# Kernel tuning notes

Hardware: AMD Instinct MI355X
Metric: run time of the kernel (lower is better)

The kernel has to match this reference:

```python
import jax, jax.numpy as jnp
import numpy as np

NUM_BANDS = 30
NUM_CH = 128
DIFF_HEAD_DIM = NUM_CH // 4 // 2  # 16
GRAPH_HEADS = 4
GRAPH_HD = NUM_CH // GRAPH_HEADS  # 32
SCALES = [2, 4, 8, 16, 32]


def _band_config():
    widths = np.array([2,3,3,3,3,3,3,3,3,3,3,8,8,8,8,8,8,8,8,8,8,8,8,16,16,16,16,16,16,16,17], dtype=np.float64)
    starts = np.concatenate([[0.0], np.cumsum(widths)])[:NUM_BANDS]
    freqs = (starts + widths[:NUM_BANDS] / 2.0) * 31.25
    slot = {2: 0, 4: 1, 8: 2, 16: 3, 32: 4}
    scale_slots, init_w = [], []
    for f in freqs:
        if f < 500:
            sc, iw = [8, 16, 32], [0.1, 0.3, 0.6]
        elif f < 2000:
            sc, iw = [4, 8, 16], [0.3, 0.4, 0.3]
        else:
            sc, iw = [2, 4, 8], [0.6, 0.3, 0.1]
        scale_slots.append([slot[s] for s in sc])
        init_w.append(iw)
    return freqs, np.array(scale_slots, np.int32), np.array(init_w, np.float32)

BAND_FREQS, SCALE_SLOTS, INIT_W = _band_config()


def setup_inputs() -> dict:
    key = jax.random.key(0)
    ks = iter(jax.random.split(key, 64))
    B, N, T, K = 4, NUM_CH, 512, NUM_BANDS

    def nrm(shape, fan):
        return jax.random.normal(next(ks), shape, jnp.float32) / np.sqrt(fan)

    inp = {}
    inp['x'] = jax.random.normal(next(ks), (B, N, T, K), jnp.float32)
    # per-band differential attention weights (stored [in, out])
    inp['Wq'] = nrm((K, N, N), N)
    inp['Wk'] = nrm((K, N, N), N)
    inp['Wv'] = nrm((K, N, N // 2), N)
    inp['Wo'] = nrm((K, N // 2, N), N // 2)
    inp['bo'] = jnp.zeros((K, N), jnp.float32)
    # per-band lambda predictors
    inp['lw1'] = nrm((K, 8, 16), 8)
    inp['lb1'] = jnp.zeros((K, 16), jnp.float32)
    inp['lw2'] = nrm((K, 16, 1), 16)
    inp['lb2'] = jnp.zeros((K, 1), jnp.float32)
    # shared multiscale conv kernels (torch OIH layout)
    for s in SCALES:
        inp[f'cw{s}'] = nrm((N, N, s), N * s)
        inp[f'cb{s}'] = jnp.zeros((N,), jnp.float32)
    inp['fusion_w'] = jnp.asarray(INIT_W)
    inp['band_embed'] = jnp.log(jnp.asarray(BAND_FREQS, jnp.float32) + 1.0)[:, None] * jax.random.normal(next(ks), (K, 64), jnp.float32) * 0.1
    # graph attention weights
    inp['gWq'] = nrm((N, N), N); inp['gbq'] = jnp.zeros((N,), jnp.float32)
    inp['gWk'] = nrm((N, N), N); inp['gbk'] = jnp.zeros((N,), jnp.float32)
    inp['gWv'] = nrm((N, N), N); inp['gbv'] = jnp.zeros((N,), jnp.float32)
    inp['gWo'] = nrm((N, N), N); inp['gbo'] = jnp.zeros((N,), jnp.float32)
    return inp


def reference(x, Wq, Wk, Wv, Wo, bo, lw1, lb1, lw2, lb2,
              cw2, cb2, cw4, cb4, cw8, cb8, cw16, cb16, cw32, cb32,
              fusion_w, band_embed, gWq, gbq, gWk, gbk, gWv, gbv, gWo, gbo):
    B, N, T, K = x.shape

    # ---- 1. Differential band attention (vectorized over the 30 bands) ----
    xb = jnp.transpose(x, (3, 0, 2, 1))                         # [K,B,T,N]
    q = jnp.einsum('kbtn,knm->kbtm', xb, Wq)
    kk = jnp.einsum('kbtn,knm->kbtm', xb, Wk)
    v = jnp.einsum('kbtn,knd->kbtd', xb, Wv)                    # [K,B,T,N/2]
    q1, q2 = jnp.split(q, 2, axis=-1)
    k1, k2 = jnp.split(kk, 2, axis=-1)
    inv = 1.0 / np.sqrt(DIFF_HEAD_DIM)
    a1 = jax.nn.softmax(jnp.einsum('kbtd,kbsd->kbts', q1, k1) * inv, axis=-1)
    a2 = jax.nn.softmax(jnp.einsum('kbtd,kbsd->kbts', q2, k2) * inv, axis=-1)

    def stats(a):  # mean / unbiased std / max / min over the [T,T] map
        return (a.mean(axis=(-2, -1)), jnp.std(a, axis=(-2, -1), ddof=1),
                a.max(axis=(-2, -1)), a.min(axis=(-2, -1)))

    st = jnp.stack(stats(a1) + stats(a2), axis=-1)              # [K,B,8]
    h = jax.nn.relu(jnp.einsum('kbi,kio->kbo', st, lw1) + lb1[:, None, :])
    lam = jax.nn.sigmoid(jnp.einsum('kbo,koj->kbj', h, lw2) + lb2[:, None, :])[..., None]  # [K,B,1,1]
    ad = a1 - lam * a2
    ob = jnp.einsum('kbts,kbsd->kbtd', ad, v)
    ob = jnp.einsum('kbtd,kdn->kbtn', ob, Wo) + bo[:, None, None, :]
    h1 = jnp.transpose(ob, (1, 3, 2, 0))                        # [B,N,T,K]

    # ---- 2. Frequency-adaptive multiscale conv fusion ----
    xm = jnp.transpose(h1, (0, 3, 1, 2)).reshape(B * K, N, T)   # bands into batch

    def conv(xc, w, b, s):
        y = jax.lax.conv_general_dilated(xc, w, (1,), [(s // 2, s // 2)],
                                         dimension_numbers=('NCH', 'OIH', 'NCH'))
        return y[:, :, :T] + b[None, :, None]                   # trim even-kernel extra frame

    co = jnp.stack([conv(xm, w, b, s) for (w, b, s) in
                    [(cw2, cb2, 2), (cw4, cb4, 4), (cw8, cb8, 8), (cw16, cb16, 16), (cw32, cb32, 32)]], 0)
    sw = jax.nn.softmax(fusion_w, axis=-1)                      # [K,3]
    Wfull = jnp.zeros((K, 5), x.dtype).at[jnp.arange(K)[:, None], jnp.asarray(SCALE_SLOTS)].set(sw)
    co = co.reshape(5, B, K, N, T)
    h2 = jnp.transpose(jnp.einsum('ks,sbknt->bknt', Wfull, co), (0, 2, 3, 1))  # [B,N,T,K]

    # ---- 3. Learnable harmonic graph attention across bands ----
    e = band_embed / (jnp.linalg.norm(band_embed, axis=-1, keepdims=True) + 1e-8)
    sim = e @ e.T
    vals, idx = jax.lax.top_k(sim, 5)
    A = jnp.zeros((K, K), x.dtype).at[jnp.arange(K)[:, None], idx].set(vals)
    A = (A + A.T) / 2
    M = B * T
    xg = jnp.transpose(h2, (0, 2, 3, 1)).reshape(M, K, N)       # [B*T, 30, 128]
    qg = jnp.transpose((xg @ gWq + gbq).reshape(M, K, GRAPH_HEADS, GRAPH_HD), (0, 2, 1, 3))
    kg = jnp.transpose((xg @ gWk + gbk).reshape(M, K, GRAPH_HEADS, GRAPH_HD), (0, 2, 1, 3))
    vg = jnp.transpose((xg @ gWv + gbv).reshape(M, K, GRAPH_HEADS, GRAPH_HD), (0, 2, 1, 3))
    sc = jnp.einsum('mhid,mhjd->mhij', qg, kg) / np.sqrt(float(GRAPH_HD))
    sc = jnp.where((A != 0)[None, None], sc, -jnp.inf)
    at = jnp.nan_to_num(jax.nn.softmax(sc, axis=-1))
    og = jnp.einsum('mhij,mhjd->mhid', at, vg)
    og = jnp.transpose(og, (0, 2, 1, 3)).reshape(M, K, N) @ gWo + gbo
    out = jnp.transpose(og.reshape(B, T, K, N), (0, 3, 1, 2))   # [B,N,T,K]
    return out
```

## Files before the change

### kernel.cpp

```cpp
#include <hip/hip_runtime.h>

typedef const float* fp;
typedef unsigned short u16;
typedef __attribute__((ext_vector_type(8))) short bf16x8;
typedef __attribute__((ext_vector_type(4))) float f32x4;

__device__ __forceinline__ u16 f2b(float f) {
  union { float f; unsigned u; } a; a.f = f;
  unsigned u = a.u;
  u += 0x7fffu + ((u >> 16) & 1u);
  return (u16)(u >> 16);
}
__device__ __forceinline__ void splitf(float x, u16& h, u16& l) {
  union { float f; unsigned u; } a; a.f = x;
  unsigned hu = a.u & 0xFFFF0000u;
  h = (u16)(hu >> 16);
  union { unsigned u; float f; } b; b.u = hu;
  l = f2b(x - b.f);
}

__global__ __launch_bounds__(64) void k_adj(fp be, float* mask) {
  __shared__ float e[30][65];
  __shared__ float sim[30][33];
  __shared__ float A[30][33];
  int tid = threadIdx.x;
  for (int idx = tid; idx < 30 * 64; idx += 64) e[idx / 64][idx % 64] = be[idx];
  __syncthreads();
  if (tid < 30) {
    float s = 0.f;
    for (int d = 0; d < 64; d++) s += e[tid][d] * e[tid][d];
    float sc = 1.0f / (sqrtf(s) + 1e-8f);
    for (int d = 0; d < 64; d++) e[tid][d] *= sc;
  }
  __syncthreads();
  if (tid < 30) {
    for (int j = 0; j < 30; j++) {
      float s = 0.f;
      for (int d = 0; d < 64; d++) s += e[tid][d] * e[j][d];
      sim[tid][j] = s;
    }
    for (int j = 0; j < 30; j++) A[tid][j] = 0.f;
  }
  __syncthreads();
  if (tid < 30) {
    unsigned used = 0;
    for (int t = 0; t < 5; t++) {
      float best = -1e30f; int bi = 0;
      for (int j = 0; j < 30; j++)
        if (!((used >> j) & 1u) && sim[tid][j] > best) { best = sim[tid][j]; bi = j; }
      A[tid][bi] = best; used |= 1u << bi;
    }
  }
  __syncthreads();
  for (int idx = tid; idx < 900; idx += 64) {
    int i = idx / 30, j = idx % 30;
    float s = A[i][j] + A[j][i];
    mask[idx] = (s != 0.0f) ? 1.0f : 0.0f;
  }
}

__global__ __launch_bounds__(128) void k_qkv(fp x, fp Wq, fp Wk, fp Wv,
                                             u16* qh, u16* ql, u16* kh, u16* kl,
                                             u16* vTh, u16* vTl) {
  int kb = blockIdx.z, b = blockIdx.y, t0 = blockIdx.x * 8;
  int tid = threadIdx.x;
  __shared__ float xs[8][129];
  for (int idx = tid; idx < 8 * 128; idx += 128) {
    int r = idx >> 7, n = idx & 127;
    xs[r][n] = x[((long)(b * 128 + n) * 512 + (t0 + r)) * 30 + kb];
  }
  __syncthreads();
  int m = tid;
  float aq[8], ak[8], av[8];
#pragma unroll
  for (int r = 0; r < 8; r++) { aq[r] = 0.f; ak[r] = 0.f; av[r] = 0.f; }
  for (int n = 0; n < 128; n++) {
    float wq = Wq[(kb * 128 + n) * 128 + m];
    float wk = Wk[(kb * 128 + n) * 128 + m];
    float wv = (m < 64) ? Wv[(kb * 128 + n) * 64 + m] : 0.f;
#pragma unroll
    for (int r = 0; r < 8; r++) {
      float xv = xs[r][n];
      aq[r] += xv * wq; ak[r] += xv * wk; av[r] += xv * wv;
    }
  }
  int pair = kb * 4 + b;
  long base = (long)pair * 512 + t0;
#pragma unroll
  for (int r = 0; r < 8; r++) {
    u16 hh, ll;
    splitf(aq[r], hh, ll); qh[(base + r) * 128 + m] = hh; ql[(base + r) * 128 + m] = ll;
    splitf(ak[r], hh, ll); kh[(base + r) * 128 + m] = hh; kl[(base + r) * 128 + m] = ll;
    if (m < 64) {
      splitf(av[r], hh, ll);
      long vo = ((long)pair * 64 + m) * 512 + t0 + r;
      vTh[vo] = hh; vTl[vo] = ll;
    }
  }
}

__global__ __launch_bounds__(256) void k_flash(const u16* qh, const u16* ql,
                                               const u16* kh, const u16* kl,
                                               const u16* vTh, const u16* vTl,
                                               float* rowstats, float* ob1, float* ob2) {
  int pair = blockIdx.y;
  int t0 = blockIdx.x * 16;
  int tid = threadIdx.x;
  int wave = tid >> 6, lane = tid & 63;
  int l15 = lane & 15, quad = lane >> 4;

  __shared__ float fbig[8704];
  __shared__ float st[2][16][4][4];
  __shared__ float fin[2][16][2];

  const long pb = (long)pair * 512 * 128;
  const u16* qhb = qh + pb; const u16* qlb = ql + pb;
  const u16* khb = kh + pb; const u16* klb = kl + pb;

  float sc[2][8][4];
#pragma unroll
  for (int h = 0; h < 2; h++) {
    long abase = (long)(t0 + l15) * 128 + h * 64 + quad * 8;
    bf16x8 Ah0 = *(const bf16x8*)(qhb + abase);
    bf16x8 Ah1 = *(const bf16x8*)(qhb + abase + 32);
    bf16x8 Al0 = *(const bf16x8*)(qlb + abase);
    bf16x8 Al1 = *(const bf16x8*)(qlb + abase + 32);
#pragma unroll
    for (int ct = 0; ct < 8; ct++) {
      int scol = wave * 128 + ct * 16 + l15;
      long bbase = (long)scol * 128 + h * 64 + quad * 8;
      bf16x8 Bh0 = *(const bf16x8*)(khb + bbase);
      bf16x8 Bh1 = *(const bf16x8*)(khb + bbase + 32);
      bf16x8 Bl0 = *(const bf16x8*)(klb + bbase);
      bf16x8 Bl1 = *(const bf16x8*)(klb + bbase + 32);
      f32x4 d = {0.f, 0.f, 0.f, 0.f};
      d = __builtin_amdgcn_mfma_f32_16x16x32_bf16(Ah0, Bh0, d, 0, 0, 0);
      d = __builtin_amdgcn_mfma_f32_16x16x32_bf16(Ah1, Bh1, d, 0, 0, 0);
      d = __builtin_amdgcn_mfma_f32_16x16x32_bf16(Ah0, Bl0, d, 0, 0, 0);
      d = __builtin_amdgcn_mfma_f32_16x16x32_bf16(Ah1, Bl1, d, 0, 0, 0);
      d = __builtin_amdgcn_mfma_f32_16x16x32_bf16(Al0, Bh0, d, 0, 0, 0);
      d = __builtin_amdgcn_mfma_f32_16x16x32_bf16(Al1, Bh1, d, 0, 0, 0);
#pragma unroll
      for (int r = 0; r < 4; r++) sc[h][ct][r] = d[r] * 0.25f;
    }
  }
#pragma unroll
  for (int h = 0; h < 2; h++)
#pragma unroll
    for (int r = 0; r < 4; r++) {
      float m = -1e30f, mnv = 1e30f;
#pragma unroll
      for (int ct = 0; ct < 8; ct++) { m = fmaxf(m, sc[h][ct][r]); mnv = fminf(mnv, sc[h][ct][r]); }
      for (int d = 1; d < 16; d <<= 1) { m = fmaxf(m, __shfl_xor(m, d)); mnv = fminf(mnv, __shfl_xor(mnv, d)); }
      float z = 0.f, s2 = 0.f;
#pragma unroll
      for (int ct = 0; ct < 8; ct++) { float e = expf(sc[h][ct][r] - m); z += e; s2 += e * e; }
      for (int d = 1; d < 16; d <<= 1) { z += __shfl_xor(z, d); s2 += __shfl_xor(s2, d); }
      if (l15 == 0) {
        st[h][quad * 4 + r][wave][0] = m;  st[h][quad * 4 + r][wave][1] = z;
        st[h][quad * 4 + r][wave][2] = s2; st[h][quad * 4 + r][wave][3] = mnv;
      }
    }
  __syncthreads();
  if (tid < 32) {
    int row = tid & 15, h = tid >> 4;
    float Mf = -1e30f, mnf = 1e30f;
    for (int w = 0; w < 4; w++) { Mf = fmaxf(Mf, st[h][row][w][0]); mnf = fminf(mnf, st[h][row][w][3]); }
    float Z = 0.f, S2 = 0.f;
    for (int w = 0; w < 4; w++) {
      float f = expf(st[h][row][w][0] - Mf);
      Z += st[h][row][w][1] * f; S2 += st[h][row][w][2] * f * f;
    }
    float* o = rowstats + ((long)pair * 512 + t0 + row) * 8 + h * 4;
    o[0] = Mf; o[1] = Z; o[2] = S2; o[3] = mnf;
    fin[h][row][0] = Mf; fin[h][row][1] = 1.0f / Z;
  }
  __syncthreads();
  u16* pbuf = (u16*)fbig;
#pragma unroll
  for (int h = 0; h < 2; h++)
#pragma unroll
    for (int r = 0; r < 4; r++) {
      int row = quad * 4 + r;
      float Mf = fin[h][row][0], iZ = fin[h][row][1];
#pragma unroll
      for (int ct = 0; ct < 8; ct++) {
        float p = expf(sc[h][ct][r] - Mf) * iZ;
        pbuf[((h * 4 + wave) * 16 + row) * 136 + ct * 16 + l15] = f2b(p);
      }
    }
  __syncthreads();
  f32x4 acc[2][4];
#pragma unroll
  for (int h = 0; h < 2; h++)
#pragma unroll
    for (int nt = 0; nt < 4; nt++) acc[h][nt] = {0.f, 0.f, 0.f, 0.f};
  const u16* vThb = vTh + (long)pair * 64 * 512;
  const u16* vTlb = vTl + (long)pair * 64 * 512;
#pragma unroll
  for (int kc = 0; kc < 4; kc++) {
    int sbase = wave * 128 + kc * 32 + quad * 8;
    bf16x8 A0 = *(const bf16x8*)(pbuf + ((0 * 4 + wave) * 16 + l15) * 136 + kc * 32 + quad * 8);
    bf16x8 A1 = *(const bf16x8*)(pbuf + ((1 * 4 + wave) * 16 + l15) * 136 + kc * 32 + quad * 8);
#pragma unroll
    for (int nt = 0; nt < 4; nt++) {
      long vo = (long)(nt * 16 + l15) * 512 + sbase;
      bf16x8 Vh = *(const bf16x8*)(vThb + vo);
      bf16x8 Vl = *(const bf16x8*)(vTlb + vo);
      acc[0][nt] = __builtin_amdgcn_mfma_f32_16x16x32_bf16(A0, Vh, acc[0][nt], 0, 0, 0);
      acc[0][nt] = __builtin_amdgcn_mfma_f32_16x16x32_bf16(A0, Vl, acc[0][nt], 0, 0, 0);
      acc[1][nt] = __builtin_amdgcn_mfma_f32_16x16x32_bf16(A1, Vh, acc[1][nt], 0, 0, 0);
      acc[1][nt] = __builtin_amdgcn_mfma_f32_16x16x32_bf16(A1, Vl, acc[1][nt], 0, 0, 0);
    }
  }
  __syncthreads();
  float* obr = fbig;
#pragma unroll
  for (int h = 0; h < 2; h++)
#pragma unroll
    for (int nt = 0; nt < 4; nt++)
#pragma unroll
      for (int r = 0; r < 4; r++)
        obr[((wave * 2 + h) * 16 + quad * 4 + r) * 68 + nt * 16 + l15] = acc[h][nt][r];
  __syncthreads();
  for (int i = tid; i < 2048; i += 256) {
    int h = i >> 10, row = (i >> 6) & 15, d = i & 63;
    float s = 0.f;
    for (int w = 0; w < 4; w++) s += obr[((w * 2 + h) * 16 + row) * 68 + d];
    float* dst = (h == 0 ? ob1 : ob2);
    dst[((long)pair * 512 + t0 + row) * 64 + d] = s;
  }
}

__global__ __launch_bounds__(64) void k_lam(const float* rowstats, fp lw1, fp lb1,
                                            fp lw2, fp lb2, float* lam) {
  int pair = blockIdx.x; int kb = pair >> 2;
  int tid = threadIdx.x;
  const float* rs = rowstats + (long)pair * 512 * 8;
  float mx1 = -1e30f, mn1 = 1e30f, ss1 = 0.f, mx2 = -1e30f, mn2 = 1e30f, ss2 = 0.f;
  for (int j = 0; j < 8; j++) {
    const float* rr = rs + (long)(j * 64 + tid) * 8;
    float M1 = rr[0], Z1 = rr[1], S21 = rr[2], m1 = rr[3];
    float M2 = rr[4], Z2 = rr[5], S22 = rr[6], m2 = rr[7];
    mx1 = fmaxf(mx1, 1.0f / Z1); mn1 = fminf(mn1, expf(m1 - M1) / Z1); ss1 += S21 / (Z1 * Z1);
    mx2 = fmaxf(mx2, 1.0f / Z2); mn2 = fminf(mn2, expf(m2 - M2) / Z2); ss2 += S22 / (Z2 * Z2);
  }
  __shared__ float red[64][8];
  red[tid][0] = mx1; red[tid][1] = mn1; red[tid][2] = ss1;
  red[tid][3] = mx2; red[tid][4] = mn2; red[tid][5] = ss2;
  __syncthreads();
  if (tid == 0) {
    for (int e = 1; e < 64; e++) {
      mx1 = fmaxf(mx1, red[e][0]); mn1 = fminf(mn1, red[e][1]); ss1 += red[e][2];
      mx2 = fmaxf(mx2, red[e][3]); mn2 = fminf(mn2, red[e][4]); ss2 += red[e][5];
    }
    const float mean = 1.0f / 512.0f;
    const float n = 262144.0f;
    float v1 = (ss1 - n * mean * mean) / (n - 1.0f); float sd1 = sqrtf(fmaxf(v1, 0.f));
    float v2 = (ss2 - n * mean * mean) / (n - 1.0f); float sd2 = sqrtf(fmaxf(v2, 0.f));
    float stv[8] = { mean, sd1, mx1, mn1, mean, sd2, mx2, mn2 };
    float acc = lb2[kb];
    for (int o = 0; o < 16; o++) {
      float h = lb1[kb * 16 + o];
      for (int i = 0; i < 8; i++) h += stv[i] * lw1[(kb * 8 + i) * 16 + o];
      h = fmaxf(h, 0.f);
      acc += h * lw2[kb * 16 + o];
    }
    lam[pair] = 1.0f / (1.0f + expf(-acc));
  }
}

__global__ __launch_bounds__(128) void k_ep(const float* ob1, const float* ob2,
                                            const float* lam, fp Wo, fp bo, float* h1) {
  int pair = blockIdx.y; int kb = pair >> 2, b = pair & 3;
  int t0 = blockIdx.x * 8;
  int tid = threadIdx.x;
  float lv = lam[pair];
  __shared__ float obs[8][68];
  for (int i = tid; i < 512; i += 128) {
    int r = i >> 6, d = i & 63;
    long o = ((long)pair * 512 + t0 + r) * 64 + d;
    obs[r][d] = ob1[o] - lv * ob2[o];
  }
  __syncthreads();
  int n = tid;
  float acc[8];
#pragma unroll
  for (int r = 0; r < 8; r++) acc[r] = bo[kb * 128 + n];
  for (int dd = 0; dd < 64; dd++) {
    float w = Wo[(kb * 64 + dd) * 128 + n];
#pragma unroll
    for (int r = 0; r < 8; r++) acc[r] += obs[r][dd] * w;
  }
#pragma unroll
  for (int r = 0; r < 8; r++)
    h1[((long)(b * 30 + kb) * 512 + t0 + r) * 128 + n] = acc[r];
}

__global__ __launch_bounds__(256) void k_ck(fp fw, fp cw2, fp cw4, fp cw8,
                                            fp cw16, fp cw32, u16* ckh, u16* ckl) {
  long idx = (long)blockIdx.x * 256 + threadIdx.x;
  int ni = idx & 127;
  int no = (idx >> 7) & 127;
  int r  = (idx >> 14) & 31;
  int kb = idx >> 19;
  float f0 = fw[kb * 3 + 0], f1 = fw[kb * 3 + 1], f2 = fw[kb * 3 + 2];
  float mx = fmaxf(f0, fmaxf(f1, f2));
  float e0 = expf(f0 - mx), e1 = expf(f1 - mx), e2 = expf(f2 - mx);
  float zi = 1.0f / (e0 + e1 + e2);
  float sw[3] = { e0 * zi, e1 * zi, e2 * zi };
  int sbase; fp cws[3];
  if (kb < 6)       { sbase = 8; cws[0] = cw8;  cws[1] = cw16; cws[2] = cw32; }
  else if (kb < 15) { sbase = 4; cws[0] = cw4;  cws[1] = cw8;  cws[2] = cw16; }
  else              { sbase = 2; cws[0] = cw2;  cws[1] = cw4;  cws[2] = cw8;  }
  float val = 0.f;
  int rs = r - 16;
#pragma unroll
  for (int j = 0; j < 3; j++) {
    int s = sbase << j;
    int tau = rs + (s >> 1);
    if (tau >= 0 && tau < s) val += sw[j] * cws[j][((long)no * 128 + ni) * s + tau];
  }
  u16 h, l; splitf(val, h, l);
  ckh[idx] = h; ckl[idx] = l;
}

__global__ __launch_bounds__(256) void k_conv(const float* h1, const u16* ckh,
                                              const u16* ckl, fp fw,
                                              fp cb2, fp cb4, fp cb8, fp cb16,
                                              fp cb32, float* h2) {
  int kb = blockIdx.z, b = blockIdx.y, t0 = blockIdx.x * 64;
  int tid = threadIdx.x;
  int wave = tid >> 6, lane = tid & 63, l15 = lane & 15, quad = lane >> 4;
  __shared__ u16 xs_h[96 * 136];
  __shared__ u16 xs_l[96 * 136];
  const float* xrow = h1 + (long)(b * 30 + kb) * 512 * 128;
  for (int i = tid; i < 3072; i += 256) {
    int row = i >> 5, c4 = (i & 31) << 2;
    int t = t0 - 16 + row;
    float4 xv = {0.f, 0.f, 0.f, 0.f};
    if (t >= 0 && t < 512) xv = *(const float4*)(xrow + (long)t * 128 + c4);
    u16 h, l;
    splitf(xv.x, h, l); xs_h[row * 136 + c4 + 0] = h; xs_l[row * 136 + c4 + 0] = l;
    splitf(xv.y, h, l); xs_h[row * 136 + c4 + 1] = h; xs_l[row * 136 + c4 + 1] = l;
    splitf(xv.z, h, l); xs_h[row * 136 + c4 + 2] = h; xs_l[row * 136 + c4 + 2] = l;
    splitf(xv.w, h, l); xs_h[row * 136 + c4 + 3] = h; xs_l[row * 136 + c4 + 3] = l;
  }
  float f0 = fw[kb * 3 + 0], f1 = fw[kb * 3 + 1], f2 = fw[kb * 3 + 2];
  float mx = fmaxf(f0, fmaxf(f1, f2));
  float e0 = expf(f0 - mx), e1 = expf(f1 - mx), e2 = expf(f2 - mx);
  float zi = 1.0f / (e0 + e1 + e2);
  float sw0 = e0 * zi, sw1 = e1 * zi, sw2 = e2 * zi;
  int rlo, rhi; fp c0, c1, c2;
  if (kb < 6)       { rlo = 0;  rhi = 32; c0 = cb8; c1 = cb16; c2 = cb32; }
  else if (kb < 15) { rlo = 8;  rhi = 24; c0 = cb4; c1 = cb8;  c2 = cb16; }
  else              { rlo = 12; rhi = 20; c0 = cb2; c1 = cb4;  c2 = cb8;  }
  __syncthreads();
  f32x4 acc[4][2];
#pragma unroll
  for (int mt = 0; mt < 4; mt++) { acc[mt][0] = {0.f,0.f,0.f,0.f}; acc[mt][1] = {0.f,0.f,0.f,0.f}; }
  for (int r = rlo; r < rhi; r++) {
    const u16* wh = ckh + ((long)(kb * 32 + r) * 128 + wave * 32 + l15) * 128;
    const u16* wl = ckl + ((long)(kb * 32 + r) * 128 + wave * 32 + l15) * 128;
#pragma unroll
    for (int c = 0; c < 4; c++) {
      int koff = c * 32 + quad * 8;
      bf16x8 Bh0 = *(const bf16x8*)(wh + koff);
      bf16x8 Bh1 = *(const bf16x8*)(wh + 2048 + koff);
      bf16x8 Bl0 = *(const bf16x8*)(wl + koff);
      bf16x8 Bl1 = *(const bf16x8*)(wl + 2048 + koff);
#pragma unroll
      for (int mt = 0; mt < 4; mt++) {
        int arow = mt * 16 + l15 + r;
        bf16x8 Ah = *(const bf16x8*)(xs_h + arow * 136 + koff);
        bf16x8 Al = *(const bf16x8*)(xs_l + arow * 136 + koff);
        acc[mt][0] = __builtin_amdgcn_mfma_f32_16x16x32_bf16(Ah, Bh0, acc[mt][0], 0, 0, 0);
        acc[mt][0] = __builtin_amdgcn_mfma_f32_16x16x32_bf16(Ah, Bl0, acc[mt][0], 0, 0, 0);
        acc[mt][0] = __builtin_amdgcn_mfma_f32_16x16x32_bf16(Al, Bh0, acc[mt][0], 0, 0, 0);
        acc[mt][1] = __builtin_amdgcn_mfma_f32_16x16x32_bf16(Ah, Bh1, acc[mt][1], 0, 0, 0);
        acc[mt][1] = __builtin_amdgcn_mfma_f32_16x16x32_bf16(Ah, Bl1, acc[mt][1], 0, 0, 0);
        acc[mt][1] = __builtin_amdgcn_mfma_f32_16x16x32_bf16(Al, Bh1, acc[mt][1], 0, 0, 0);
      }
    }
  }
  int no0 = wave * 32 + l15;
  float bias0 = sw0 * c0[no0] + sw1 * c1[no0] + sw2 * c2[no0];
  float bias1 = sw0 * c0[no0 + 16] + sw1 * c1[no0 + 16] + sw2 * c2[no0 + 16];
#pragma unroll
  for (int mt = 0; mt < 4; mt++)
#pragma unroll
    for (int reg = 0; reg < 4; reg++) {
      int t = t0 + mt * 16 + quad * 4 + reg;
      long ob = ((long)(b * 512 + t) * 30 + kb) * 128 + no0;
      h2[ob] = acc[mt][0][reg] + bias0;
      h2[ob + 16] = acc[mt][1][reg] + bias1;
    }
}

__global__ __launch_bounds__(128) void k_gqkv(const float* h2, fp gWq, fp gbq,
                                              fp gWk, fp gbk, fp gWv, fp gbv,
                                              float* qg, float* kg, float* vg) {
  long row0 = (long)blockIdx.x * 16;
  int m = threadIdx.x;
  __shared__ float xs[16][132];
  for (int idx = m; idx < 16 * 128; idx += 128) {
    int r = idx >> 7, c = idx & 127;
    xs[r][c] = h2[(row0 + r) * 128 + c];
  }
  __syncthreads();
  float aq[16], ak[16], av[16];
#pragma unroll
  for (int r = 0; r < 16; r++) { aq[r] = 0.f; ak[r] = 0.f; av[r] = 0.f; }
  for (int n = 0; n < 128; n++) {
    float wq = gWq[n * 128 + m], wk = gWk[n * 128 + m], wv = gWv[n * 128 + m];
#pragma unroll
    for (int r = 0; r < 16; r++) {
      float xv = xs[r][n];
      aq[r] += xv * wq; ak[r] += xv * wk; av[r] += xv * wv;
    }
  }
  float bq = gbq[m], bk = gbk[m], bv = gbv[m];
#pragma unroll
  for (int r = 0; r < 16; r++) {
    qg[(row0 + r) * 128 + m] = aq[r] + bq;
    kg[(row0 + r) * 128 + m] = ak[r] + bk;
    vg[(row0 + r) * 128 + m] = av[r] + bv;
  }
}

__global__ __launch_bounds__(128) void k_gattn(const float* qg, const float* kg,
                                               const float* vg, const float* maskw,
                                               fp gWo, fp gbo, float* out) {
  int m = blockIdx.x; int b = m >> 9; int t = m & 511;
  int tid = threadIdx.x;
  __shared__ float qs[30][132];
  __shared__ float ks[30][132];
  __shared__ float vs[30][132];
  __shared__ float msk[30][32];
  float (*ogs)[132] = qs;
  const float* qb = qg + (long)m * 30 * 128;
  const float* kb2 = kg + (long)m * 30 * 128;
  const float* vb2 = vg + (long)m * 30 * 128;
  for (int idx = tid; idx < 3840; idx += 128) {
    int j = idx >> 7, n = idx & 127;
    qs[j][n] = qb[idx]; ks[j][n] = kb2[idx]; vs[j][n] = vb2[idx];
  }
  for (int idx = tid; idx < 900; idx += 128) msk[idx / 30][idx % 30] = maskw[idx];
  __syncthreads();
  float p[30]; float iZ = 0.f; int hi = 0, ii = 0;
  if (tid < 120) {
    hi = tid / 30; ii = tid % 30;
    int hb = hi * 32;
    float4 qv[8];
#pragma unroll
    for (int dq = 0; dq < 8; dq++) qv[dq] = *(const float4*)&qs[ii][hb + dq * 4];
    float mx = -1e30f;
#pragma unroll
    for (int j = 0; j < 30; j++) {
      float s = 0.f;
      const float4* kr = (const float4*)&ks[j][hb];
#pragma unroll
      for (int dq = 0; dq < 8; dq++) {
        float4 kv = kr[dq];
        s += qv[dq].x * kv.x + qv[dq].y * kv.y + qv[dq].z * kv.z + qv[dq].w * kv.w;
      }
      s *= 0.17677669529663687f;
      p[j] = (msk[ii][j] != 0.f) ? s : -1e30f;
      mx = fmaxf(mx, p[j]);
    }
    float Z = 0.f;
#pragma unroll
    for (int j = 0; j < 30; j++) { float e = expf(p[j] - mx); p[j] = e; Z += e; }
    iZ = 1.0f / Z;
  }
  __syncthreads();
  if (tid < 120) {
    int hb = hi * 32;
#pragma unroll
    for (int dq = 0; dq < 8; dq++) {
      float sx = 0.f, sy = 0.f, sz = 0.f, sw2 = 0.f;
#pragma unroll
      for (int j = 0; j < 30; j++) {
        float4 vv = *(const float4*)&vs[j][hb + dq * 4];
        sx += p[j] * vv.x; sy += p[j] * vv.y; sz += p[j] * vv.z; sw2 += p[j] * vv.w;
      }
      float4 o = { sx * iZ, sy * iZ, sz * iZ, sw2 * iZ };
      *(float4*)&ogs[ii][hb + dq * 4] = o;
    }
  }
  __syncthreads();
  {
    int n = tid;
    float acc[30];
#pragma unroll
    for (int j = 0; j < 30; j++) acc[j] = 0.f;
    for (int d = 0; d < 128; d += 4) {
      float w0 = gWo[(d + 0) * 128 + n];
      float w1 = gWo[(d + 1) * 128 + n];
      float w2 = gWo[(d + 2) * 128 + n];
      float w3 = gWo[(d + 3) * 128 + n];
#pragma unroll
      for (int j = 0; j < 30; j++) {
        float4 og4 = *(const float4*)&ogs[j][d];
        acc[j] += og4.x * w0 + og4.y * w1 + og4.z * w2 + og4.w * w3;
      }
    }
    float gb = gbo[n];
    float* outp = out + ((long)(b * 128 + n) * 512 + t) * 30;
#pragma unroll
    for (int j = 0; j < 30; j++) outp[j] = acc[j] + gb;
  }
}

extern "C" void kernel_launch(void* const* d_in, const int* in_sizes, int n_in,
                              void* d_out, int out_size, void* d_ws, size_t ws_size,
                              hipStream_t stream) {
  fp x = (fp)d_in[0], Wq = (fp)d_in[1], Wk = (fp)d_in[2], Wv = (fp)d_in[3],
     Wo = (fp)d_in[4], bo = (fp)d_in[5], lw1 = (fp)d_in[6], lb1 = (fp)d_in[7],
     lw2 = (fp)d_in[8], lb2 = (fp)d_in[9],
     cw2 = (fp)d_in[10], cb2 = (fp)d_in[11], cw4 = (fp)d_in[12], cb4 = (fp)d_in[13],
     cw8 = (fp)d_in[14], cb8 = (fp)d_in[15], cw16 = (fp)d_in[16], cb16 = (fp)d_in[17],
     cw32 = (fp)d_in[18], cb32 = (fp)d_in[19], fw = (fp)d_in[20], be = (fp)d_in[21],
     gWq = (fp)d_in[22], gbq = (fp)d_in[23], gWk = (fp)d_in[24], gbk = (fp)d_in[25],
     gWv = (fp)d_in[26], gbv = (fp)d_in[27], gWo = (fp)d_in[28], gbo = (fp)d_in[29];
  (void)in_sizes; (void)n_in; (void)out_size; (void)ws_size;

  float* ws = (float*)d_ws;
  u16* qh  = (u16*)ws;
  u16* ql  = (u16*)(ws + 3932160L);
  u16* kh  = (u16*)(ws + 7864320L);
  u16* kl  = (u16*)(ws + 11796480L);
  u16* vTh = (u16*)(ws + 15728640L);
  u16* vTl = (u16*)(ws + 17694720L);
  float* rowstats = ws + 19660800L;
  float* lam      = ws + 20152320L;
  float* ob1 = ws;
  float* ob2 = ws + 3932160L;
  float* h1  = ws + 23592960L;
  u16* ckh = (u16*)ws;
  u16* ckl = (u16*)(ws + 7864320L);
  float* h2  = ws + 15728640L;
  float* qg  = ws;
  float* kg  = ws + 7864320L;
  float* vg  = ws + 23592960L;
  float* maskw = ws + 31457280L;

  k_adj<<<1, 64, 0, stream>>>(be, maskw);
  k_qkv<<<dim3(64, 4, 30), 128, 0, stream>>>(x, Wq, Wk, Wv, qh, ql, kh, kl, vTh, vTl);
  k_flash<<<dim3(32, 120), 256, 0, stream>>>(qh, ql, kh, kl, vTh, vTl, rowstats, ob1, ob2);
  k_lam<<<120, 64, 0, stream>>>(rowstats, lw1, lb1, lw2, lb2, lam);
  k_ep<<<dim3(64, 120), 128, 0, stream>>>(ob1, ob2, lam, Wo, bo, h1);
  k_ck<<<61440, 256, 0, stream>>>(fw, cw2, cw4, cw8, cw16, cw32, ckh, ckl);
  k_conv<<<dim3(8, 4, 30), 256, 0, stream>>>(h1, ckh, ckl, fw, cb2, cb4, cb8, cb16, cb32, h2);
  k_gqkv<<<3840, 128, 0, stream>>>(h2, gWq, gbq, gWk, gbk, gWv, gbv, qg, kg, vg);
  k_gattn<<<2048, 128, 0, stream>>>(qg, kg, vg, maskw, gWo, gbo, (float*)d_out);
}
```

Baseline: 966.9 us.

## Move band QKV and graph projections to split-bf16 MFMA, fuse graph QKV into attention

The band Q/K/V projection and the graph Q/K/V/O projections move from scalar FP32 FMA loops to MFMA with a three-term bf16 hi/lo split. For this, weights are pre-transposed and pre-split by two new small kernels, and the conv writes h2 as split bf16. The graph QKV kernel is fused into the graph attention kernel, so the qg/kg/vg round trip through memory goes away. The flash kernel reuses the exps computed during the row-stat pass instead of recomputing them. The conv-kernel prep now only builds the taps each band actually uses, shrinking the k_ck grid. All of this adds extra launches and a workspace relayout, and the split-bf16 products are slightly less precise than FP32.

New measurement: 882.1 us. -8.8%, faster.

```diff
diff --git a/kernel.cpp b/kernel.cpp
--- a/kernel.cpp
+++ b/kernel.cpp
@@ -59,42 +59,105 @@
   }
 }
 
-__global__ __launch_bounds__(128) void k_qkv(fp x, fp Wq, fp Wk, fp Wv,
+__global__ __launch_bounds__(256) void k_wt_band(fp Wq, fp Wk, fp Wv, u16* wh, u16* wl) {
+  int kb = blockIdx.x, which = blockIdx.y;
+  __shared__ float wsb[128][129];
+  int tid = threadIdx.x;
+  int M = (which == 2) ? 64 : 128;
+  int sh = (which == 2) ? 6 : 7;
+  fp src = (which == 0) ? (Wq + kb * 16384) : (which == 1) ? (Wk + kb * 16384) : (Wv + kb * 8192);
+  for (int i = tid; i < 128 * M; i += 256) {
+    int n = i >> sh, m = i & (M - 1);
+    wsb[n][m] = src[i];
+  }
+  __syncthreads();
+  long base = (long)kb * 40960 + which * 16384;
+  for (int o = tid; o < 128 * M; o += 256) {
+    int m = o >> 7, n = o & 127;
+    u16 h, l; splitf(wsb[n][m], h, l);
+    wh[base + m * 128 + n] = h; wl[base + m * 128 + n] = l;
+  }
+}
+
+__global__ __launch_bounds__(256) void k_wt_graph(fp gWq, fp gWk, fp gWv, fp gWo,
+                                                  u16* wh, u16* wl) {
+  int w = blockIdx.x;
+  fp src = (w == 0) ? gWq : (w == 1) ? gWk : (w == 2) ? gWv : gWo;
+  __shared__ float wsb[128][129];
+  int tid = threadIdx.x;
+  for (int i = tid; i < 16384; i += 256) wsb[i >> 7][i & 127] = src[i];
+  __syncthreads();
+  long base = (long)w * 16384;
+  for (int o = tid; o < 16384; o += 256) {
+    int m = o >> 7, n = o & 127;
+    u16 h, l; splitf(wsb[n][m], h, l);
+    wh[base + m * 128 + n] = h; wl[base + m * 128 + n] = l;
+  }
+}
+
+__global__ __launch_bounds__(256) void k_qkv(fp x, const u16* wh, const u16* wl,
                                              u16* qh, u16* ql, u16* kh, u16* kl,
                                              u16* vTh, u16* vTl) {
-  int kb = blockIdx.z, b = blockIdx.y, t0 = blockIdx.x * 8;
-  int tid = threadIdx.x;
-  __shared__ float xs[8][129];
-  for (int idx = tid; idx < 8 * 128; idx += 128) {
-    int r = idx >> 7, n = idx & 127;
-    xs[r][n] = x[((long)(b * 128 + n) * 512 + (t0 + r)) * 30 + kb];
-  }
-  __syncthreads();
-  int m = tid;
-  float aq[8], ak[8], av[8];
-#pragma unroll
-  for (int r = 0; r < 8; r++) { aq[r] = 0.f; ak[r] = 0.f; av[r] = 0.f; }
-  for (int n = 0; n < 128; n++) {
-    float wq = Wq[(kb * 128 + n) * 128 + m];
-    float wk = Wk[(kb * 128 + n) * 128 + m];
-    float wv = (m < 64) ? Wv[(kb * 128 + n) * 64 + m] : 0.f;
-#pragma unroll
-    for (int r = 0; r < 8; r++) {
-      float xv = xs[r][n];
-      aq[r] += xv * wq; ak[r] += xv * wk; av[r] += xv * wv;
-    }
+  int kb = blockIdx.z, b = blockIdx.y, t0 = blockIdx.x * 64;
+  int tid = threadIdx.x;
+  int wave = tid >> 6, lane = tid & 63, l15 = lane & 15, quad = lane >> 4;
+  __shared__ u16 xs_h[64 * 136];
+  __shared__ u16 xs_l[64 * 136];
+  for (int i = tid; i < 8192; i += 256) {
+    int tl = i >> 7, n = i & 127;
+    float v = x[((long)(b * 128 + n) * 512 + t0 + tl) * 30 + kb];
+    u16 h, l; splitf(v, h, l);
+    xs_h[tl * 136 + n] = h; xs_l[tl * 136 + n] = l;
+  }
+  __syncthreads();
+  int arow = wave * 16 + l15;
+  bf16x8 Ah[4], Al[4];
+#pragma unroll
+  for (int kc = 0; kc < 4; kc++) {
+    Ah[kc] = *(const bf16x8*)(xs_h + arow * 136 + kc * 32 + quad * 8);
+    Al[kc] = *(const bf16x8*)(xs_l + arow * 136 + kc * 32 + quad * 8);
   }
   int pair = kb * 4 + b;
-  long base = (long)pair * 512 + t0;
-#pragma unroll
-  for (int r = 0; r < 8; r++) {
-    u16 hh, ll;
-    splitf(aq[r], hh, ll); qh[(base + r) * 128 + m] = hh; ql[(base + r) * 128 + m] = ll;
-    splitf(ak[r], hh, ll); kh[(base + r) * 128 + m] = hh; kl[(base + r) * 128 + m] = ll;
-    if (m < 64) {
-      splitf(av[r], hh, ll);
-      long vo = ((long)pair * 64 + m) * 512 + t0 + r;
-      vTh[vo] = hh; vTl[vo] = ll;
+  const u16* wbh = wh + (long)kb * 40960;
+  const u16* wbl = wl + (long)kb * 40960;
+  for (int c = 0; c < 20; c++) {
+    f32x4 d = {0.f, 0.f, 0.f, 0.f};
+#pragma unroll
+    for (int kc = 0; kc < 4; kc++) {
+      long boff = (long)(c * 16 + l15) * 128 + kc * 32 + quad * 8;
+      bf16x8 Bh = *(const bf16x8*)(wbh + boff);
+      bf16x8 Bl = *(const bf16x8*)(wbl + boff);
+      d = __builtin_amdgcn_mfma_f32_16x16x32_bf16(Ah[kc], Bh, d, 0, 0, 0);
+      d = __builtin_amdgcn_mfma_f32_16x16x32_bf16(Ah[kc], Bl, d, 0, 0, 0);
+      d = __builtin_amdgcn_mfma_f32_16x16x32_bf16(Al[kc], Bh, d, 0, 0, 0);
+    }
+    if (c < 8) {
+      int m = c * 16 + l15;
+#pragma unroll
+      for (int r = 0; r < 4; r++) {
+        int trow = t0 + wave * 16 + quad * 4 + r;
+        u16 h, l; splitf(d[r], h, l);
+        long o = ((long)pair * 512 + trow) * 128 + m;
+        qh[o] = h; ql[o] = l;
+      }
+    } else if (c < 16) {
+      int m = (c - 8) * 16 + l15;
+#pragma unroll
+      for (int r = 0; r < 4; r++) {
+        int trow = t0 + wave * 16 + quad * 4 + r;
+        u16 h, l; splitf(d[r], h, l);
+        long o = ((long)pair * 512 + trow) * 128 + m;
+        kh[o] = h; kl[o] = l;
+      }
+    } else {
+      int dcol = (c - 16) * 16 + l15;
+#pragma unroll
+      for (int r = 0; r < 4; r++) {
+        int trow = t0 + wave * 16 + quad * 4 + r;
+        u16 h, l; splitf(d[r], h, l);
+        long o = ((long)pair * 64 + dcol) * 512 + trow;
+        vTh[o] = h; vTl[o] = l;
+      }
     }
   }
 }
@@ -118,6 +181,7 @@
   const u16* khb = kh + pb; const u16* klb = kl + pb;
 
   float sc[2][8][4];
+  float mw[2][4];
 #pragma unroll
   for (int h = 0; h < 2; h++) {
     long abase = (long)(t0 + l15) * 128 + h * 64 + quad * 8;
@@ -154,8 +218,12 @@
       for (int d = 1; d < 16; d <<= 1) { m = fmaxf(m, __shfl_xor(m, d)); mnv = fminf(mnv, __shfl_xor(mnv, d)); }
       float z = 0.f, s2 = 0.f;
 #pragma unroll
-      for (int ct = 0; ct < 8; ct++) { float e = expf(sc[h][ct][r] - m); z += e; s2 += e * e; }
+      for (int ct = 0; ct < 8; ct++) {
+        float e = expf(sc[h][ct][r] - m); z += e; s2 += e * e;
+        sc[h][ct][r] = e;
+      }
       for (int d = 1; d < 16; d <<= 1) { z += __shfl_xor(z, d); s2 += __shfl_xor(s2, d); }
+      mw[h][r] = m;
       if (l15 == 0) {
         st[h][quad * 4 + r][wave][0] = m;  st[h][quad * 4 + r][wave][1] = z;
         st[h][quad * 4 + r][wave][2] = s2; st[h][quad * 4 + r][wave][3] = mnv;
@@ -182,10 +250,10 @@
 #pragma unroll
     for (int r = 0; r < 4; r++) {
       int row = quad * 4 + r;
-      float Mf = fin[h][row][0], iZ = fin[h][row][1];
+      float scale = expf(mw[h][r] - fin[h][row][0]) * fin[h][row][1];
 #pragma unroll
       for (int ct = 0; ct < 8; ct++) {
-        float p = expf(sc[h][ct][r] - Mf) * iZ;
+        float p = sc[h][ct][r] * scale;
         pbuf[((h * 4 + wave) * 16 + row) * 136 + ct * 16 + l15] = f2b(p);
       }
     }
@@ -302,8 +370,11 @@
   long idx = (long)blockIdx.x * 256 + threadIdx.x;
   int ni = idx & 127;
   int no = (idx >> 7) & 127;
-  int r  = (idx >> 14) & 31;
-  int kb = idx >> 19;
+  int g  = (int)(idx >> 14);
+  int kb, r;
+  if (g < 192)      { kb = g >> 5;                r = g & 31; }
+  else if (g < 336) { int gg = g - 192; kb = 6 + (gg >> 4);  r = 8 + (gg & 15); }
+  else              { int gg = g - 336; kb = 15 + (gg >> 3); r = 12 + (gg & 7); }
   float f0 = fw[kb * 3 + 0], f1 = fw[kb * 3 + 1], f2 = fw[kb * 3 + 2];
   float mx = fmaxf(f0, fmaxf(f1, f2));
   float e0 = expf(f0 - mx), e1 = expf(f1 - mx), e2 = expf(f2 - mx);
@@ -328,7 +399,7 @@
 __global__ __launch_bounds__(256) void k_conv(const float* h1, const u16* ckh,
                                               const u16* ckl, fp fw,
                                               fp cb2, fp cb4, fp cb8, fp cb16,
-                                              fp cb32, float* h2) {
+                                              fp cb32, u16* h2h, u16* h2l) {
   int kb = blockIdx.z, b = blockIdx.y, t0 = blockIdx.x * 64;
   int tid = threadIdx.x;
   int wave = tid >> 6, lane = tid & 63, l15 = lane & 15, quad = lane >> 4;
@@ -351,17 +422,17 @@
   float e0 = expf(f0 - mx), e1 = expf(f1 - mx), e2 = expf(f2 - mx);
   float zi = 1.0f / (e0 + e1 + e2);
   float sw0 = e0 * zi, sw1 = e1 * zi, sw2 = e2 * zi;
-  int rlo, rhi; fp c0, c1, c2;
-  if (kb < 6)       { rlo = 0;  rhi = 32; c0 = cb8; c1 = cb16; c2 = cb32; }
-  else if (kb < 15) { rlo = 8;  rhi = 24; c0 = cb4; c1 = cb8;  c2 = cb16; }
-  else              { rlo = 12; rhi = 20; c0 = cb2; c1 = cb4;  c2 = cb8;  }
+  int rlo, rhi, gbase; fp c0, c1, c2;
+  if (kb < 6)       { rlo = 0;  rhi = 32; gbase = kb * 32;            c0 = cb8; c1 = cb16; c2 = cb32; }
+  else if (kb < 15) { rlo = 8;  rhi = 24; gbase = 192 + (kb - 6) * 16;  c0 = cb4; c1 = cb8;  c2 = cb16; }
+  else              { rlo = 12; rhi = 20; gbase = 336 + (kb - 15) * 8;  c0 = cb2; c1 = cb4;  c2 = cb8;  }
   __syncthreads();
   f32x4 acc[4][2];
 #pragma unroll
   for (int mt = 0; mt < 4; mt++) { acc[mt][0] = {0.f,0.f,0.f,0.f}; acc[mt][1] = {0.f,0.f,0.f,0.f}; }
   for (int r = rlo; r < rhi; r++) {
-    const u16* wh = ckh + ((long)(kb * 32 + r) * 128 + wave * 32 + l15) * 128;
-    const u16* wl = ckl + ((long)(kb * 32 + r) * 128 + wave * 32 + l15) * 128;
+    const u16* wh = ckh + ((long)(gbase + r - rlo) * 128 + wave * 32 + l15) * 128;
+    const u16* wl = ckl + ((long)(gbase + r - rlo) * 128 + wave * 32 + l15) * 128;
 #pragma unroll
     for (int c = 0; c < 4; c++) {
       int koff = c * 32 + quad * 8;
@@ -392,61 +463,65 @@
     for (int reg = 0; reg < 4; reg++) {
       int t = t0 + mt * 16 + quad * 4 + reg;
       long ob = ((long)(b * 512 + t) * 30 + kb) * 128 + no0;
-      h2[ob] = acc[mt][0][reg] + bias0;
-      h2[ob + 16] = acc[mt][1][reg] + bias1;
-    }
-}
-
-__global__ __launch_bounds__(128) void k_gqkv(const float* h2, fp gWq, fp gbq,
-                                              fp gWk, fp gbk, fp gWv, fp gbv,
-                                              float* qg, float* kg, float* vg) {
-  long row0 = (long)blockIdx.x * 16;
-  int m = threadIdx.x;
-  __shared__ float xs[16][132];
-  for (int idx = m; idx < 16 * 128; idx += 128) {
-    int r = idx >> 7, c = idx & 127;
-    xs[r][c] = h2[(row0 + r) * 128 + c];
-  }
-  __syncthreads();
-  float aq[16], ak[16], av[16];
-#pragma unroll
-  for (int r = 0; r < 16; r++) { aq[r] = 0.f; ak[r] = 0.f; av[r] = 0.f; }
-  for (int n = 0; n < 128; n++) {
-    float wq = gWq[n * 128 + m], wk = gWk[n * 128 + m], wv = gWv[n * 128 + m];
-#pragma unroll
-    for (int r = 0; r < 16; r++) {
-      float xv = xs[r][n];
-      aq[r] += xv * wq; ak[r] += xv * wk; av[r] += xv * wv;
-    }
-  }
-  float bq = gbq[m], bk = gbk[m], bv = gbv[m];
-#pragma unroll
-  for (int r = 0; r < 16; r++) {
-    qg[(row0 + r) * 128 + m] = aq[r] + bq;
-    kg[(row0 + r) * 128 + m] = ak[r] + bk;
-    vg[(row0 + r) * 128 + m] = av[r] + bv;
-  }
-}
-
-__global__ __launch_bounds__(128) void k_gattn(const float* qg, const float* kg,
-                                               const float* vg, const float* maskw,
-                                               fp gWo, fp gbo, float* out) {
+      u16 h, l;
+      splitf(acc[mt][0][reg] + bias0, h, l); h2h[ob] = h;      h2l[ob] = l;
+      splitf(acc[mt][1][reg] + bias1, h, l); h2h[ob + 16] = h; h2l[ob + 16] = l;
+    }
+}
+
+__global__ __launch_bounds__(256) void k_gattn(const u16* h2h, const u16* h2l,
+                                               const u16* gwh, const u16* gwl,
+                                               const float* maskw,
+                                               fp gbq, fp gbk, fp gbv, fp gbo,
+                                               float* out) {
   int m = blockIdx.x; int b = m >> 9; int t = m & 511;
   int tid = threadIdx.x;
-  __shared__ float qs[30][132];
-  __shared__ float ks[30][132];
-  __shared__ float vs[30][132];
-  __shared__ float msk[30][32];
-  float (*ogs)[132] = qs;
-  const float* qb = qg + (long)m * 30 * 128;
-  const float* kb2 = kg + (long)m * 30 * 128;
-  const float* vb2 = vg + (long)m * 30 * 128;
-  for (int idx = tid; idx < 3840; idx += 128) {
-    int j = idx >> 7, n = idx & 127;
-    qs[j][n] = qb[idx]; ks[j][n] = kb2[idx]; vs[j][n] = vb2[idx];
-  }
-  for (int idx = tid; idx < 900; idx += 128) msk[idx / 30][idx % 30] = maskw[idx];
-  __syncthreads();
+  int wave = tid >> 6, lane = tid & 63, l15 = lane & 15, quad = lane >> 4;
+  __shared__ float qs[32][136];
+  __shared__ float ks[32][136];
+  __shared__ float vs[32][136];
+  u16* ogs_h = (u16*)&qs[0][0];
+  u16* ogs_l = ogs_h + 32 * 136;
+
+  {
+    int mtile = wave & 1;
+    int c0 = (wave >> 1) * 12;
+    long abase0 = (long)m * 30 * 128;
+    bf16x8 Ah[4], Al[4];
+    bf16x8 zero8 = {0, 0, 0, 0, 0, 0, 0, 0};
+    int row = mtile * 16 + l15;
+#pragma unroll
+    for (int kc = 0; kc < 4; kc++) {
+      if (row < 30) {
+        Ah[kc] = *(const bf16x8*)(h2h + abase0 + (long)row * 128 + kc * 32 + quad * 8);
+        Al[kc] = *(const bf16x8*)(h2l + abase0 + (long)row * 128 + kc * 32 + quad * 8);
+      } else { Ah[kc] = zero8; Al[kc] = zero8; }
+    }
+    for (int cc = 0; cc < 12; cc++) {
+      int c = c0 + cc;
+      f32x4 d = {0.f, 0.f, 0.f, 0.f};
+#pragma unroll
+      for (int kc = 0; kc < 4; kc++) {
+        long boff = (long)(c * 16 + l15) * 128 + kc * 32 + quad * 8;
+        bf16x8 Bh = *(const bf16x8*)(gwh + boff);
+        bf16x8 Bl = *(const bf16x8*)(gwl + boff);
+        d = __builtin_amdgcn_mfma_f32_16x16x32_bf16(Ah[kc], Bh, d, 0, 0, 0);
+        d = __builtin_amdgcn_mfma_f32_16x16x32_bf16(Ah[kc], Bl, d, 0, 0, 0);
+        d = __builtin_amdgcn_mfma_f32_16x16x32_bf16(Al[kc], Bh, d, 0, 0, 0);
+      }
+      int region = c >> 3;
+      int ch = (c & 7) * 16 + l15;
+      float bias = (region == 0) ? gbq[ch] : (region == 1) ? gbk[ch] : gbv[ch];
+      float (*dst)[136] = (region == 0) ? qs : (region == 1) ? ks : vs;
+#pragma unroll
+      for (int r = 0; r < 4; r++) {
+        int rowo = mtile * 16 + quad * 4 + r;
+        if (rowo < 30) dst[rowo][ch] = d[r] + bias;
+      }
+    }
+  }
+  __syncthreads();
+
   float p[30]; float iZ = 0.f; int hi = 0, ii = 0;
   if (tid < 120) {
     hi = tid / 30; ii = tid % 30;
@@ -465,7 +540,7 @@
         s += qv[dq].x * kv.x + qv[dq].y * kv.y + qv[dq].z * kv.z + qv[dq].w * kv.w;
       }
       s *= 0.17677669529663687f;
-      p[j] = (msk[ii][j] != 0.f) ? s : -1e30f;
+      p[j] = (maskw[ii * 30 + j] != 0.f) ? s : -1e30f;
       mx = fmaxf(mx, p[j]);
     }
     float Z = 0.f;
@@ -484,31 +559,48 @@
         float4 vv = *(const float4*)&vs[j][hb + dq * 4];
         sx += p[j] * vv.x; sy += p[j] * vv.y; sz += p[j] * vv.z; sw2 += p[j] * vv.w;
       }
-      float4 o = { sx * iZ, sy * iZ, sz * iZ, sw2 * iZ };
-      *(float4*)&ogs[ii][hb + dq * 4] = o;
-    }
-  }
-  __syncthreads();
+      float o4[4] = { sx * iZ, sy * iZ, sz * iZ, sw2 * iZ };
+#pragma unroll
+      for (int cpt = 0; cpt < 4; cpt++) {
+        u16 h, l; splitf(o4[cpt], h, l);
+        ogs_h[ii * 136 + hb + dq * 4 + cpt] = h;
+        ogs_l[ii * 136 + hb + dq * 4 + cpt] = l;
+      }
+    }
+  }
+  __syncthreads();
+
   {
-    int n = tid;
-    float acc[30];
-#pragma unroll
-    for (int j = 0; j < 30; j++) acc[j] = 0.f;
-    for (int d = 0; d < 128; d += 4) {
-      float w0 = gWo[(d + 0) * 128 + n];
-      float w1 = gWo[(d + 1) * 128 + n];
-      float w2 = gWo[(d + 2) * 128 + n];
-      float w3 = gWo[(d + 3) * 128 + n];
-#pragma unroll
-      for (int j = 0; j < 30; j++) {
-        float4 og4 = *(const float4*)&ogs[j][d];
-        acc[j] += og4.x * w0 + og4.y * w1 + og4.z * w2 + og4.w * w3;
-      }
-    }
-    float gb = gbo[n];
-    float* outp = out + ((long)(b * 128 + n) * 512 + t) * 30;
-#pragma unroll
-    for (int j = 0; j < 30; j++) outp[j] = acc[j] + gb;
+    int mtile = wave & 1;
+    int nc0 = (wave >> 1) * 4;
+    int row = mtile * 16 + l15;
+    bf16x8 Ah[4], Al[4];
+#pragma unroll
+    for (int kc = 0; kc < 4; kc++) {
+      Ah[kc] = *(const bf16x8*)(ogs_h + row * 136 + kc * 32 + quad * 8);
+      Al[kc] = *(const bf16x8*)(ogs_l + row * 136 + kc * 32 + quad * 8);
+    }
+    for (int cc = 0; cc < 4; cc++) {
+      int nchunk = nc0 + cc;
+      f32x4 d = {0.f, 0.f, 0.f, 0.f};
+#pragma unroll
+      for (int kc = 0; kc < 4; kc++) {
+        long boff = (long)(384 + nchunk * 16 + l15) * 128 + kc * 32 + quad * 8;
+        bf16x8 Bh = *(const bf16x8*)(gwh + boff);
+        bf16x8 Bl = *(const bf16x8*)(gwl + boff);
+        d = __builtin_amdgcn_mfma_f32_16x16x32_bf16(Ah[kc], Bh, d, 0, 0, 0);
+        d = __builtin_amdgcn_mfma_f32_16x16x32_bf16(Ah[kc], Bl, d, 0, 0, 0);
+        d = __builtin_amdgcn_mfma_f32_16x16x32_bf16(Al[kc], Bh, d, 0, 0, 0);
+      }
+      int n = nchunk * 16 + l15;
+      float gb = gbo[n];
+      long obase = ((long)(b * 128 + n) * 512 + t) * 30;
+#pragma unroll
+      for (int r = 0; r < 4; r++) {
+        int kbo = mtile * 16 + quad * 4 + r;
+        if (kbo < 30) out[obase + kbo] = d[r] + gb;
+      }
+    }
   }
 }
 
@@ -534,24 +626,27 @@
   u16* vTl = (u16*)(ws + 17694720L);
   float* rowstats = ws + 19660800L;
   float* lam      = ws + 20152320L;
-  float* ob1 = ws;
-  float* ob2 = ws + 3932160L;
-  float* h1  = ws + 23592960L;
-  u16* ckh = (u16*)ws;
-  u16* ckl = (u16*)(ws + 7864320L);
-  float* h2  = ws + 15728640L;
-  float* qg  = ws;
-  float* kg  = ws + 7864320L;
-  float* vg  = ws + 23592960L;
-  float* maskw = ws + 31457280L;
+  u16* wqkT_h = (u16*)(ws + 20152448L);
+  u16* wqkT_l = (u16*)(ws + 20766848L);
+  u16* gwT_h  = (u16*)(ws + 21381248L);
+  u16* gwT_l  = (u16*)(ws + 21414016L);
+  float* maskw = ws + 21446784L;
+  float* ob1 = ws + 21447808L;
+  float* ob2 = ws + 25379968L;
+  float* h1  = ws;
+  u16* h2h = (u16*)(ws + 7864320L);
+  u16* h2l = (u16*)(ws + 11796480L);
+  u16* ckh = (u16*)(ws + 21447808L);
+  u16* ckl = (u16*)(ws + 25183360L);
 
   k_adj<<<1, 64, 0, stream>>>(be, maskw);
-  k_qkv<<<dim3(64, 4, 30), 128, 0, stream>>>(x, Wq, Wk, Wv, qh, ql, kh, kl, vTh, vTl);
+  k_wt_band<<<dim3(30, 3), 256, 0, stream>>>(Wq, Wk, Wv, wqkT_h, wqkT_l);
+  k_wt_graph<<<4, 256, 0, stream>>>(gWq, gWk, gWv, gWo, gwT_h, gwT_l);
+  k_qkv<<<dim3(8, 4, 30), 256, 0, stream>>>(x, wqkT_h, wqkT_l, qh, ql, kh, kl, vTh, vTl);
   k_flash<<<dim3(32, 120), 256, 0, stream>>>(qh, ql, kh, kl, vTh, vTl, rowstats, ob1, ob2);
   k_lam<<<120, 64, 0, stream>>>(rowstats, lw1, lb1, lw2, lb2, lam);
   k_ep<<<dim3(64, 120), 128, 0, stream>>>(ob1, ob2, lam, Wo, bo, h1);
-  k_ck<<<61440, 256, 0, stream>>>(fw, cw2, cw4, cw8, cw16, cw32, ckh, ckl);
-  k_conv<<<dim3(8, 4, 30), 256, 0, stream>>>(h1, ckh, ckl, fw, cb2, cb4, cb8, cb16, cb32, h2);
-  k_gqkv<<<3840, 128, 0, stream>>>(h2, gWq, gbq, gWk, gbk, gWv, gbv, qg, kg, vg);
-  k_gattn<<<2048, 128, 0, stream>>>(qg, kg, vg, maskw, gWo, gbo, (float*)d_out);
-}
+  k_ck<<<29184, 256, 0, stream>>>(fw, cw2, cw4, cw8, cw16, cw32, ckh, ckl);
+  k_conv<<<dim3(8, 4, 30), 256, 0, stream>>>(h1, ckh, ckl, fw, cb2, cb4, cb8, cb16, cb32, h2h, h2l);
+  k_gattn<<<2048, 256, 0, stream>>>(h2h, h2l, gwT_h, gwT_l, maskw, gbq, gbk, gbv, gbo, (float*)d_out);
+}
```
